# Optimization experiments

Hardware: AMD Instinct MI355X
Metric: run time of the kernel (lower is better)

## Reference

```python
import jax, jax.numpy as jnp
import numpy as np
import math

INPUT_FRAMES = 12
FUTURE_FRAMES = 26
T_STEPS = INPUT_FRAMES + FUTURE_FRAMES - 1  # 37
HD = 64   # hidden_dim
D = 16    # d_attn
CIN = 3   # input channels (time='stable')
COUT = 2  # output_dim
H, W = 24, 48


def conv2d(x, w, b, pad):
    # x: (N,C,H,W), w: (O,I,kh,kw)
    y = jax.lax.conv_general_dilated(x, w, (1, 1), [(pad, pad), (pad, pad)],
                                     dimension_numbers=('NCHW', 'OIHW', 'NCHW'))
    return y + b[None, :, None, None]


def spatial_attn(q, k, v):
    # q,k,v: (N,C,S); attention over spatial dim S
    scale = 1.0 / math.sqrt(q.shape[1])
    scores = jnp.einsum('ncs,nct->nst', q, k) * scale  # (N,S,S)
    a = jax.nn.softmax(scores, axis=-1)
    return jnp.einsum('nst,nct->ncs', a, v)


def setup_inputs() -> dict:
    key = jax.random.key(0)
    ks = jax.random.split(key, 8)
    s = 0.05
    inp = {
        'input_x': jax.random.normal(ks[0], (16, T_STEPS, H, W, CIN), dtype=jnp.float32),
        # ConvLSTM gate conv: in = CIN+HD, out = 4*HD, 3x3
        'conv_w': jax.random.normal(ks[1], (4 * HD, CIN + HD, 3, 3), dtype=jnp.float32) * s,
        'conv_b': jnp.zeros((4 * HD,), jnp.float32),
        # SA memory module
        'h_w': jax.random.normal(ks[2], (3 * D, HD, 1, 1), dtype=jnp.float32) * s,
        'h_b': jnp.zeros((3 * D,), jnp.float32),
        'm_w': jax.random.normal(ks[3], (2 * D, HD, 1, 1), dtype=jnp.float32) * s,
        'm_b': jnp.zeros((2 * D,), jnp.float32),
        'z_w': jax.random.normal(ks[4], (D, 2 * D, 1, 1), dtype=jnp.float32) * s,
        'z_b': jnp.zeros((D,), jnp.float32),
        'o_w': jax.random.normal(ks[5], (3 * HD, HD + D, 3, 3), dtype=jnp.float32) * s,
        'o_b': jnp.zeros((3 * HD,), jnp.float32),
        # final 1x1 projection to output_dim
        'out_w': jax.random.normal(ks[6], (COUT, HD, 1, 1), dtype=jnp.float32) * s,
        'out_b': jnp.zeros((COUT,), jnp.float32),
    }
    return inp


def reference(input_x, conv_w, conv_b, h_w, h_b, m_w, m_b, z_w, z_b, o_w, o_b, out_w, out_b):
    x = jnp.transpose(input_x, (0, 1, 4, 2, 3))  # (N,T,C,H,W)
    N = x.shape[0]
    S = H * W

    h0 = jnp.zeros((N, HD, H, W), x.dtype)
    carry0 = (h0, h0, h0, jnp.zeros((N, COUT, H, W), x.dtype))

    def step(carry, inp_t):
        h, c, m, prev_out = carry
        xt, t = inp_t  # xt: (N,CIN,H,W), t: scalar
        autoreg = jnp.concatenate([prev_out, xt[:, 2:]], axis=1)
        feed = jnp.where(t < INPUT_FRAMES, xt, autoreg)
        # ConvLSTM gates
        comb = conv2d(jnp.concatenate([feed, h], axis=1), conv_w, conv_b, 1)
        ci, cf, co, cg = jnp.split(comb, 4, axis=1)
        i = jax.nn.sigmoid(ci)
        f = jax.nn.sigmoid(cf)
        o = jax.nn.sigmoid(co)
        g = jnp.tanh(cg)
        c = f * c + i * g
        h = o * jnp.tanh(c)
        # self-attention memory
        hq, hk, hv = jnp.split(conv2d(h, h_w, h_b, 0), 3, axis=1)
        mk, mv = jnp.split(conv2d(m, m_w, m_b, 0), 2, axis=1)
        Zh = spatial_attn(hq.reshape(N, D, S), hk.reshape(N, D, S), hv.reshape(N, D, S))
        Zm = spatial_attn(hq.reshape(N, D, S), mk.reshape(N, D, S), mv.reshape(N, D, S))
        Z = conv2d(jnp.concatenate([Zh.reshape(N, D, H, W), Zm.reshape(N, D, H, W)], axis=1), z_w, z_b, 0)
        iog = conv2d(jnp.concatenate([Z, h], axis=1), o_w, o_b, 1)
        si, sg, so = jnp.split(iog, 3, axis=1)
        si = jax.nn.sigmoid(si)
        sg = jnp.tanh(sg)
        m = si * sg + (1.0 - si) * m
        h = jax.nn.sigmoid(so) * m
        out = conv2d(h, out_w, out_b, 0)
        return (h, c, m, out), out

    xs = (jnp.transpose(x, (1, 0, 2, 3, 4)), jnp.arange(T_STEPS))
    _, outs = jax.lax.scan(step, carry0, xs)
    outputs = jnp.transpose(outs, (1, 0, 2, 3, 4))  # (N,T,COUT,H,W)

    nino = outputs[:, -FUTURE_FRAMES:, 0, 10:13, 19:30].mean(axis=(2, 3))  # (N,26)
    nino_pred = (nino[:, :-2] + nino[:, 1:-1] + nino[:, 2:]) / 3.0          # (N,24)
    return outputs, nino_pred
```

## Files before the change

kernel.cpp:

```cpp
#include <hip/hip_runtime.h>
#include <math.h>

#define HD 64
#define DATT 16
#define NCIN 3
#define NCOUT 2
#define HH 24
#define WW 48
#define SS (HH*WW)
#define NB 16
#define TSTEPS 37
#define INPUT_FRAMES 12

#define PR 26
#define PC 52
#define PHW (PR*PC)

#define OFF_H     0
#define OFF_C     1384448
#define OFF_M     2564096
#define OFF_FEED  3743744
#define OFF_Z     3808640
#define ZERO_END  4154752
#define OFF_QKV   4154752
#define OFF_MKV   5039488
#define OFF_HB    5629312
#define OFF_IOG   8873344
#define OFF_BF2   12412288
#define OFF_BF    12596864

typedef __attribute__((ext_vector_type(8))) short short8;
typedef __attribute__((ext_vector_type(4))) float f32x4;

__device__ __forceinline__ float sigmoidf_(float x) {
    return 1.0f / (1.0f + __expf(-x));
}
__device__ __forceinline__ unsigned short f2bf(float f) {
    unsigned u = __float_as_uint(f);
    unsigned r = (u + 0x7fffu + ((u >> 16) & 1u)) >> 16;
    return (unsigned short)r;
}
__device__ __forceinline__ float bf2f(unsigned short b) {
    return __uint_as_float(((unsigned)b) << 16);
}
__device__ __forceinline__ unsigned packbf(float f) {
    unsigned short hi = f2bf(f);
    unsigned short lo = f2bf(f - bf2f(hi));
    return ((unsigned)lo << 16) | (unsigned)hi;
}
__device__ __forceinline__ float unpackbf(unsigned pk) {
    return __uint_as_float(pk << 16) + __uint_as_float(pk & 0xffff0000u);
}
__device__ __forceinline__ unsigned cvt_pk_bf16(float a, float b) {
    unsigned r;
    asm("v_cvt_pk_bf16_f32 %0, %1, %2" : "=v"(r) : "v"(a), "v"(b));
    return r;
}
__device__ __forceinline__ int permrow(int t) {
    int kb = t >> 5, tl = t & 31;
    int quad = tl >> 3, rr = tl & 7;
    return kb * 32 + ((rr >= 4) ? 16 : 0) + quad * 4 + (rr & 3);
}

#define MKFRAG(P0, P1, ah, al) do {                                  \
    ah.i[0] = (P0.y << 16) | (P0.x & 0xffff);                        \
    ah.i[1] = (P0.w << 16) | (P0.z & 0xffff);                        \
    ah.i[2] = (P1.y << 16) | (P1.x & 0xffff);                        \
    ah.i[3] = (P1.w << 16) | (P1.z & 0xffff);                        \
    al.i[0] = (P0.y & 0xffff0000) | ((unsigned)P0.x >> 16);          \
    al.i[1] = (P0.w & 0xffff0000) | ((unsigned)P0.z >> 16);          \
    al.i[2] = (P1.y & 0xffff0000) | ((unsigned)P1.x >> 16);          \
    al.i[3] = (P1.w & 0xffff0000) | ((unsigned)P1.z >> 16);          \
} while (0)

__global__ void k_zero(float* __restrict__ p, int n4) {
    int i = blockIdx.x * blockDim.x + threadIdx.x;
    if (i < n4) ((float4*)p)[i] = make_float4(0.f, 0.f, 0.f, 0.f);
}

__global__ void k_prep_bf2(const float* __restrict__ cw, unsigned short* __restrict__ bbuf) {
    int idx = blockIdx.x * 256 + threadIdx.x;
    if (idx >= 344064) return;
    int j    = idx & 7;
    int lane = (idx >> 3) & 63;
    int ki   = (idx >> 9) % 21;
    int nt   = (idx / 10752) % 16;
    int p    = idx / 172032;
    int k = ki * 32 + (lane >> 4) * 8 + j;
    int ncol = nt * 16 + (lane & 15);
    unsigned short v = 0;
    if (k < 648) {
        int c = k % 72, kt = k / 72;
        if (c < 67) {
            float w = cw[ncol * 603 + c * 9 + kt];
            unsigned short hi = f2bf(w);
            v = (p == 0) ? hi : f2bf(w - bf2f(hi));
        }
    }
    bbuf[idx] = v;
}

__global__ void k_prep_bf(const float* __restrict__ ow, unsigned short* __restrict__ bbuf) {
    int idx = blockIdx.x * 256 + threadIdx.x;
    if (idx >= 282624) return;
    int j    = idx & 7;
    int lane = (idx >> 3) & 63;
    int ki   = (idx >> 9) % 23;
    int nt   = (idx / 11776) % 12;
    int p    = idx / 141312;
    int k = ki * 32 + (lane >> 4) * 8 + j;
    int ncol = nt * 16 + (lane & 15);
    unsigned short v = 0;
    if (k < 720) {
        int c = k % 80, kt = k / 80;
        float w = ow[ncol * 720 + c * 9 + kt];
        unsigned short hi = f2bf(w);
        v = (p == 0) ? hi : f2bf(w - bf2f(hi));
    }
    bbuf[idx] = v;
}

__global__ void k_feed0(const float* __restrict__ x, unsigned* __restrict__ feed) {
    int i = blockIdx.x * blockDim.x + threadIdx.x;
    if (i >= NB * 3 * SS) return;
    int s = i % SS;
    int ch = (i / SS) % 3;
    int n = i / (3 * SS);
    int y = s / WW, xx = s % WW;
    float v = x[(((size_t)(n * TSTEPS + 0) * HH + y) * WW + xx) * NCIN + ch];
    feed[((size_t)(n * 3 + ch) * PR + (y + 1)) * PC + (xx + 1)] = packbf(v);
}

#define ASTR2 76
#define ZOFF2 (3*52*ASTR2)
__global__ __launch_bounds__(256) void k_conv_lstm_mfma(
    const unsigned* __restrict__ feed, const unsigned* __restrict__ hin,
    const unsigned short* __restrict__ bbuf, const float* __restrict__ cb,
    float* __restrict__ c, unsigned* __restrict__ hout)
{
    __shared__ __align__(16) int lds[3 * 52 * ASTR2 + 8];
    const int y0 = blockIdx.x;
    const int nb = blockIdx.y;
    const int n  = blockIdx.z;
    const int tid = threadIdx.x;

    const int ech = tid & 31;
    const int exg = tid >> 5;
    const int egch = nb * 32 + ech;
    const size_t ecbase = ((size_t)(n * HD + egch) * HH + y0) * WW + exg * 6;
    float cpre[6];
#pragma unroll
    for (int k = 0; k < 6; ++k) cpre[k] = c[ecbase + k];
    const float ebi = cb[egch], ebf = cb[64 + egch];
    const float ebo = cb[128 + egch], ebg = cb[192 + egch];

    const unsigned* fbase = feed + (size_t)n * 3 * PHW;
    const unsigned* hbase = hin + (size_t)n * HD * PHW;
    for (int e = tid; e < 2808; e += 256) {
        int grp = e / 156;
        int r2  = e - grp * 156;
        int pr = r2 / 52, pc = r2 - pr * 52;
        int cc0 = grp * 4;
        int vv[4];
#pragma unroll
        for (int j = 0; j < 4; ++j) {
            int cc = cc0 + j;
            int t = 0;
            if (cc < 3)        t = (int)fbase[(size_t)cc * PHW + (y0 + pr) * PC + pc];
            else if (cc < 67)  t = (int)hbase[(size_t)(cc - 3) * PHW + (y0 + pr) * PC + pc];
            vv[j] = t;
        }
        int4 v; v.x = vv[0]; v.y = vv[1]; v.z = vv[2]; v.w = vv[3];
        *(int4*)&lds[r2 * ASTR2 + cc0] = v;
    }
    if (tid < 8) lds[ZOFF2 + tid] = 0;
    __syncthreads();

    const int wv = tid >> 6;
    const int lane = tid & 63;
    const int mcol = lane & 15;
    const int quad = lane >> 4;

    f32x4 acc[2][3];
#pragma unroll
    for (int jg = 0; jg < 2; ++jg)
#pragma unroll
        for (int xt = 0; xt < 3; ++xt) acc[jg][xt] = (f32x4){0.f, 0.f, 0.f, 0.f};

    const unsigned short* b0 = bbuf + ((size_t)(wv * 4 + nb * 2 + 0) * 21) * 512 + lane * 8;
    const unsigned short* b1 = bbuf + ((size_t)(wv * 4 + nb * 2 + 1) * 21) * 512 + lane * 8;

    short8 cb0h = *(const short8*)(b0);
    short8 cb0l = *(const short8*)(b0 + 172032);
    short8 cb1h = *(const short8*)(b1);
    short8 cb1l = *(const short8*)(b1 + 172032);

    for (int ki = 0; ki < 21; ++ki) {
        int kn = (ki < 20) ? (ki + 1) * 512 : 20 * 512;
        short8 nb0h = *(const short8*)(b0 + kn);
        short8 nb0l = *(const short8*)(b0 + kn + 172032);
        short8 nb1h = *(const short8*)(b1 + kn);
        short8 nb1l = *(const short8*)(b1 + kn + 172032);

        int k0 = ki * 32 + quad * 8;
        int ab, step;
        if (k0 < 648) {
            int kt = k0 / 72;
            int c0 = k0 - kt * 72;
            int dy = kt / 3, dx = kt - dy * 3;
            ab = (dy * 52 + mcol + dx) * ASTR2 + c0;
            step = 16 * ASTR2;
        } else {
            ab = ZOFF2; step = 0;
        }
        int4 A0 = *(const int4*)&lds[ab],            A1 = *(const int4*)&lds[ab + 4];
        int4 B0 = *(const int4*)&lds[ab + step],     B1 = *(const int4*)&lds[ab + step + 4];
        int4 C0 = *(const int4*)&lds[ab + 2 * step], C1 = *(const int4*)&lds[ab + 2 * step + 4];

        union { int i[4]; short8 v; } ah, al;
        MKFRAG(A0, A1, ah, al);
        acc[0][0] = __builtin_amdgcn_mfma_f32_16x16x32_bf16(ah.v, cb0h, acc[0][0], 0, 0, 0);
        acc[0][0] = __builtin_amdgcn_mfma_f32_16x16x32_bf16(ah.v, cb0l, acc[0][0], 0, 0, 0);
        acc[0][0] = __builtin_amdgcn_mfma_f32_16x16x32_bf16(al.v, cb0h, acc[0][0], 0, 0, 0);
        acc[1][0] = __builtin_amdgcn_mfma_f32_16x16x32_bf16(ah.v, cb1h, acc[1][0], 0, 0, 0);
        acc[1][0] = __builtin_amdgcn_mfma_f32_16x16x32_bf16(ah.v, cb1l, acc[1][0], 0, 0, 0);
        acc[1][0] = __builtin_amdgcn_mfma_f32_16x16x32_bf16(al.v, cb1h, acc[1][0], 0, 0, 0);
        MKFRAG(B0, B1, ah, al);
        acc[0][1] = __builtin_amdgcn_mfma_f32_16x16x32_bf16(ah.v, cb0h, acc[0][1], 0, 0, 0);
        acc[0][1] = __builtin_amdgcn_mfma_f32_16x16x32_bf16(ah.v, cb0l, acc[0][1], 0, 0, 0);
        acc[0][1] = __builtin_amdgcn_mfma_f32_16x16x32_bf16(al.v, cb0h, acc[0][1], 0, 0, 0);
        acc[1][1] = __builtin_amdgcn_mfma_f32_16x16x32_bf16(ah.v, cb1h, acc[1][1], 0, 0, 0);
        acc[1][1] = __builtin_amdgcn_mfma_f32_16x16x32_bf16(ah.v, cb1l, acc[1][1], 0, 0, 0);
        acc[1][1] = __builtin_amdgcn_mfma_f32_16x16x32_bf16(al.v, cb1h, acc[1][1], 0, 0, 0);
        MKFRAG(C0, C1, ah, al);
        acc[0][2] = __builtin_amdgcn_mfma_f32_16x16x32_bf16(ah.v, cb0h, acc[0][2], 0, 0, 0);
        acc[0][2] = __builtin_amdgcn_mfma_f32_16x16x32_bf16(ah.v, cb0l, acc[0][2], 0, 0, 0);
        acc[0][2] = __builtin_amdgcn_mfma_f32_16x16x32_bf16(al.v, cb0h, acc[0][2], 0, 0, 0);
        acc[1][2] = __builtin_amdgcn_mfma_f32_16x16x32_bf16(ah.v, cb1h, acc[1][2], 0, 0, 0);
        acc[1][2] = __builtin_amdgcn_mfma_f32_16x16x32_bf16(ah.v, cb1l, acc[1][2], 0, 0, 0);
        acc[1][2] = __builtin_amdgcn_mfma_f32_16x16x32_bf16(al.v, cb1h, acc[1][2], 0, 0, 0);

        cb0h = nb0h; cb0l = nb0l; cb1h = nb1h; cb1l = nb1l;
    }

    __syncthreads();
    float* exch = (float*)lds;
#pragma unroll
    for (int jg = 0; jg < 2; ++jg)
#pragma unroll
        for (int xt = 0; xt < 3; ++xt)
#pragma unroll
            for (int r = 0; r < 4; ++r)
                exch[((wv * 2 + jg) * 3 + xt) * 272 + (quad * 4 + r) * 17 + mcol] = acc[jg][xt][r];
    __syncthreads();

    const int jg = ech >> 4, col = ech & 15;
    unsigned* hp = hout + ((size_t)(n * HD + egch) * PR + y0 + 1) * PC + 1;
#pragma unroll
    for (int k = 0; k < 6; ++k) {
        int x = exg * 6 + k;
        int xt = x >> 4, row = x & 15;
        float iv = sigmoidf_(exch[((0 * 2 + jg) * 3 + xt) * 272 + row * 17 + col] + ebi);
        float fv = sigmoidf_(exch[((1 * 2 + jg) * 3 + xt) * 272 + row * 17 + col] + ebf);
        float ov = sigmoidf_(exch[((2 * 2 + jg) * 3 + xt) * 272 + row * 17 + col] + ebo);
        float gv = tanhf    (exch[((3 * 2 + jg) * 3 + xt) * 272 + row * 17 + col] + ebg);
        float cn = fv * cpre[k] + iv * gv;
        float hn = ov * tanhf(cn);
        c[ecbase + k] = cn;
        hp[x] = packbf(hn);
    }
}

#define ASTR (84)
#define ZOFF (3*52*ASTR)
__global__ __launch_bounds__(192) void k_conv_sa(
    const unsigned* __restrict__ Zin, const unsigned* __restrict__ hin,
    const unsigned short* __restrict__ bbuf, const float* __restrict__ ob,
    float* __restrict__ m, unsigned* __restrict__ hout)
{
    __shared__ __align__(16) int lds[3 * 52 * ASTR + 8];
    const int y0 = blockIdx.x;
    const int cbk = blockIdx.y;
    const int n  = blockIdx.z;
    const int tid = threadIdx.x;

    const int ech = tid & 31;
    const int exg = tid >> 5;
    const int egch = cbk * 32 + ech;
    float* emrow = m + ((size_t)(n * HD + egch) * HH + y0) * WW;
    float mpre[8];
    {
        float4 a = *(const float4*)&emrow[exg * 8];
        float4 b = *(const float4*)&emrow[exg * 8 + 4];
        mpre[0] = a.x; mpre[1] = a.y; mpre[2] = a.z; mpre[3] = a.w;
        mpre[4] = b.x; mpre[5] = b.y; mpre[6] = b.z; mpre[7] = b.w;
    }
    const float ebsi = ob[egch], ebsg = ob[64 + egch], ebso = ob[128 + egch];

    const unsigned* zbase = Zin + (size_t)n * DATT * PHW;
    const unsigned* hbase = hin + (size_t)n * HD * PHW;
    for (int e = tid; e < 3120; e += 192) {
        int grp = e / 156;
        int r2  = e - grp * 156;
        int pr = r2 / 52, pc = r2 - pr * 52;
        int cc0 = grp * 4;
        int vv[4];
#pragma unroll
        for (int j = 0; j < 4; ++j) {
            int cc = cc0 + j;
            const unsigned* src = (cc < 16) ? (zbase + (size_t)cc * PHW)
                                            : (hbase + (size_t)(cc - 16) * PHW);
            vv[j] = (int)src[(y0 + pr) * PC + pc];
        }
        int4 v; v.x = vv[0]; v.y = vv[1]; v.z = vv[2]; v.w = vv[3];
        *(int4*)&lds[r2 * ASTR + cc0] = v;
    }
    if (tid < 8) lds[ZOFF + tid] = 0;
    __syncthreads();

    const int wv = tid >> 6;
    const int lane = tid & 63;
    const int mcol = lane & 15;
    const int quad = lane >> 4;

    f32x4 acc[2][3];
#pragma unroll
    for (int j = 0; j < 2; ++j)
#pragma unroll
        for (int xt = 0; xt < 3; ++xt) acc[j][xt] = (f32x4){0.f, 0.f, 0.f, 0.f};

    const unsigned short* b0 = bbuf + ((size_t)(wv * 4 + cbk * 2 + 0) * 23) * 512 + lane * 8;
    const unsigned short* b1 = bbuf + ((size_t)(wv * 4 + cbk * 2 + 1) * 23) * 512 + lane * 8;

    short8 cb0h = *(const short8*)(b0);
    short8 cb0l = *(const short8*)(b0 + 141312);
    short8 cb1h = *(const short8*)(b1);
    short8 cb1l = *(const short8*)(b1 + 141312);

    for (int ki = 0; ki < 23; ++ki) {
        int kn = (ki < 22) ? (ki + 1) * 512 : 22 * 512;
        short8 nb0h = *(const short8*)(b0 + kn);
        short8 nb0l = *(const short8*)(b0 + kn + 141312);
        short8 nb1h = *(const short8*)(b1 + kn);
        short8 nb1l = *(const short8*)(b1 + kn + 141312);

        int k0 = ki * 32 + quad * 8;
        int ab, step;
        if (k0 < 720) {
            int kt = k0 / 80;
            int c0 = k0 - kt * 80;
            int dy = kt / 3, dx = kt - dy * 3;
            ab = (dy * 52 + mcol + dx) * ASTR + c0;
            step = 16 * ASTR;
        } else {
            ab = ZOFF; step = 0;
        }
        int4 A0 = *(const int4*)&lds[ab],            A1 = *(const int4*)&lds[ab + 4];
        int4 B0 = *(const int4*)&lds[ab + step],     B1 = *(const int4*)&lds[ab + step + 4];
        int4 C0 = *(const int4*)&lds[ab + 2 * step], C1 = *(const int4*)&lds[ab + 2 * step + 4];

        union { int i[4]; short8 v; } ah, al;
        MKFRAG(A0, A1, ah, al);
        acc[0][0] = __builtin_amdgcn_mfma_f32_16x16x32_bf16(ah.v, cb0h, acc[0][0], 0, 0, 0);
        acc[0][0] = __builtin_amdgcn_mfma_f32_16x16x32_bf16(ah.v, cb0l, acc[0][0], 0, 0, 0);
        acc[0][0] = __builtin_amdgcn_mfma_f32_16x16x32_bf16(al.v, cb0h, acc[0][0], 0, 0, 0);
        acc[1][0] = __builtin_amdgcn_mfma_f32_16x16x32_bf16(ah.v, cb1h, acc[1][0], 0, 0, 0);
        acc[1][0] = __builtin_amdgcn_mfma_f32_16x16x32_bf16(ah.v, cb1l, acc[1][0], 0, 0, 0);
        acc[1][0] = __builtin_amdgcn_mfma_f32_16x16x32_bf16(al.v, cb1h, acc[1][0], 0, 0, 0);
        MKFRAG(B0, B1, ah, al);
        acc[0][1] = __builtin_amdgcn_mfma_f32_16x16x32_bf16(ah.v, cb0h, acc[0][1], 0, 0, 0);
        acc[0][1] = __builtin_amdgcn_mfma_f32_16x16x32_bf16(ah.v, cb0l, acc[0][1], 0, 0, 0);
        acc[0][1] = __builtin_amdgcn_mfma_f32_16x16x32_bf16(al.v, cb0h, acc[0][1], 0, 0, 0);
        acc[1][1] = __builtin_amdgcn_mfma_f32_16x16x32_bf16(ah.v, cb1h, acc[1][1], 0, 0, 0);
        acc[1][1] = __builtin_amdgcn_mfma_f32_16x16x32_bf16(ah.v, cb1l, acc[1][1], 0, 0, 0);
        acc[1][1] = __builtin_amdgcn_mfma_f32_16x16x32_bf16(al.v, cb1h, acc[1][1], 0, 0, 0);
        MKFRAG(C0, C1, ah, al);
        acc[0][2] = __builtin_amdgcn_mfma_f32_16x16x32_bf16(ah.v, cb0h, acc[0][2], 0, 0, 0);
        acc[0][2] = __builtin_amdgcn_mfma_f32_16x16x32_bf16(ah.v, cb0l, acc[0][2], 0, 0, 0);
        acc[0][2] = __builtin_amdgcn_mfma_f32_16x16x32_bf16(al.v, cb0h, acc[0][2], 0, 0, 0);
        acc[1][2] = __builtin_amdgcn_mfma_f32_16x16x32_bf16(ah.v, cb1h, acc[1][2], 0, 0, 0);
        acc[1][2] = __builtin_amdgcn_mfma_f32_16x16x32_bf16(ah.v, cb1l, acc[1][2], 0, 0, 0);
        acc[1][2] = __builtin_amdgcn_mfma_f32_16x16x32_bf16(al.v, cb1h, acc[1][2], 0, 0, 0);

        cb0h = nb0h; cb0l = nb0l; cb1h = nb1h; cb1l = nb1l;
    }

    __syncthreads();
    float* exch = (float*)lds;
#pragma unroll
    for (int j = 0; j < 2; ++j)
#pragma unroll
        for (int xt = 0; xt < 3; ++xt)
#pragma unroll
            for (int r = 0; r < 4; ++r)
                exch[((wv * 2 + j) * 3 + xt) * 272 + (quad * 4 + r) * 17 + mcol] = acc[j][xt][r];
    __syncthreads();

    const int jg = ech >> 4, col = ech & 15;
    unsigned* hp = hout + ((size_t)(n * HD + egch) * PR + y0 + 1) * PC + 1;
#pragma unroll
    for (int k = 0; k < 8; ++k) {
        int x = exg * 8 + k;
        int xt = x >> 4, row = x & 15;
        float si = sigmoidf_(exch[((0 * 2 + jg) * 3 + xt) * 272 + row * 17 + col] + ebsi);
        float sg = tanhf    (exch[((1 * 2 + jg) * 3 + xt) * 272 + row * 17 + col] + ebsg);
        float so =           exch[((2 * 2 + jg) * 3 + xt) * 272 + row * 17 + col] + ebso;
        float mn = si * sg + (1.f - si) * mpre[k];
        emrow[x] = mn;
        hp[x] = packbf(sigmoidf_(so) * mn);
    }
}

__global__ __launch_bounds__(256) void k_qkv(
    const unsigned* __restrict__ h, const float* __restrict__ m,
    const float* __restrict__ hw, const float* __restrict__ hb,
    const float* __restrict__ mw, const float* __restrict__ mb,
    unsigned short* __restrict__ pl) {
    __shared__ float lw[512];
    __shared__ float lb[8];
    const int g = blockIdx.y;
    const int tid = threadIdx.x;
    const float* wsrc = (g < 6) ? (hw + g * 512) : (mw + (g - 6) * 512);
    const float* bsrc = (g < 6) ? (hb + g * 8) : (mb + (g - 6) * 8);
    for (int i = tid; i < 512; i += 256) lw[i] = wsrc[i];
    if (tid < 8) lb[tid] = bsrc[tid];
    __syncthreads();

    int idx = blockIdx.x * 256 + tid;
    int s = idx % SS;
    int n = idx / SS;

    float reg[HD];
    if (g < 6) {
        int y = s / WW, x = s % WW;
        const unsigned* src = h + (size_t)n * HD * PHW + (y + 1) * PC + (x + 1);
#pragma unroll
        for (int ic = 0; ic < HD; ++ic) reg[ic] = unpackbf(src[ic * PHW]);
    } else {
        const float* src = m + (size_t)n * HD * SS + s;
#pragma unroll
        for (int ic = 0; ic < HD; ++ic) reg[ic] = src[ic * SS];
    }

    float out[8];
#pragma unroll
    for (int j = 0; j < 8; ++j) {
        const float* wr = &lw[j * HD];
        float a = lb[j];
#pragma unroll
        for (int ic = 0; ic < HD; ++ic) a += reg[ic] * wr[ic];
        out[j] = a;
    }

    unsigned short* bq  = pl;
    unsigned short* akh = pl + 294912;
    unsigned short* akm = pl + 589824;
    unsigned short* bvh = pl + 884736;
    unsigned short* bvm = pl + 1179648;
    const int c0 = (g & 1) * 8;

    if (g < 2) {
        unsigned w0 = (unsigned)f2bf(out[0]) | ((unsigned)f2bf(out[1]) << 16);
        unsigned w1 = (unsigned)f2bf(out[2]) | ((unsigned)f2bf(out[3]) << 16);
        unsigned w2 = (unsigned)f2bf(out[4]) | ((unsigned)f2bf(out[5]) << 16);
        unsigned w3 = (unsigned)f2bf(out[6]) | ((unsigned)f2bf(out[7]) << 16);
        *(uint4*)&bq[((size_t)n * SS + s) * 16 + c0] = make_uint4(w0, w1, w2, w3);
    } else if (g < 4 || (g >= 6 && g < 8)) {
        int row = permrow(s);
        unsigned short* base = (g < 4) ? akh : akm;
        unsigned w0 = (unsigned)f2bf(out[0]) | ((unsigned)f2bf(out[1]) << 16);
        unsigned w1 = (unsigned)f2bf(out[2]) | ((unsigned)f2bf(out[3]) << 16);
        unsigned w2 = (unsigned)f2bf(out[4]) | ((unsigned)f2bf(out[5]) << 16);
        unsigned w3 = (unsigned)f2bf(out[6]) | ((unsigned)f2bf(out[7]) << 16);
        *(uint4*)&base[((size_t)n * SS + row) * 16 + c0] = make_uint4(w0, w1, w2, w3);
    } else {
        unsigned short* base = (g < 6) ? bvh : bvm;
#pragma unroll
        for (int j = 0; j < 8; ++j)
            base[((size_t)n * 16 + c0 + j) * SS + s] = f2bf(out[j]);
    }
}

__global__ __launch_bounds__(256) void k_attn(
    const unsigned short* __restrict__ pl, const unsigned short* __restrict__ zbuf,
    const float* __restrict__ zw, const float* __restrict__ zb,
    unsigned* __restrict__ Z)
{
    __shared__ float ldsO[4][2][16][16];
    __shared__ float ldsF[2][16][16];
    __shared__ float ldsL[4][2][16];
    __shared__ float ldsLF[2][16];

    const int n   = blockIdx.x;
    const int qt  = blockIdx.y;
    const int tid = threadIdx.x;
    const int wv  = tid >> 6;
    const int lane = tid & 63;
    const int col  = lane & 15;
    const int quad = lane >> 4;
    const bool hi  = quad >= 2;

    const unsigned short* bq  = pl;
    const unsigned short* akh = pl + 294912;
    const unsigned short* akm = pl + 589824;
    const unsigned short* bvh = pl + 884736;
    const unsigned short* bvm = pl + 1179648;

    const size_t nb = (size_t)n * 18432;
    const int stepk = hi ? 0 : 512;
    const int subk  = hi ? 0 : 256;
    const unsigned short* qp  = hi ? zbuf : (bq  + nb + ((size_t)(qt * 16 + col)) * 16 + quad * 8);
    const unsigned short* khb = hi ? zbuf : (akh + nb + col * 16 + quad * 8);
    const unsigned short* kmb = hi ? zbuf : (akm + nb + col * 16 + quad * 8);
    const unsigned short* vhb = bvh + nb + (size_t)col * SS + quad * 8;
    const unsigned short* vmb = bvm + nb + (size_t)col * SS + quad * 8;

    short8 qf = *(const short8*)qp;

    f32x4 oh = (f32x4){0.f,0.f,0.f,0.f}, om = (f32x4){0.f,0.f,0.f,0.f};
    float lh = 0.f, lm = 0.f;
    const int kb0 = wv * 9, kb1 = kb0 + 9;
    for (int kb = kb0; kb < kb1; ++kb) {
        const unsigned short* kh0 = khb + (size_t)kb * stepk;
        const unsigned short* km0 = kmb + (size_t)kb * stepk;
        short8 khA = *(const short8*)kh0;
        short8 khB = *(const short8*)(kh0 + subk);
        short8 kmA = *(const short8*)km0;
        short8 kmB = *(const short8*)(km0 + subk);
        short8 vh  = *(const short8*)(vhb + (size_t)kb * 32);
        short8 vm  = *(const short8*)(vmb + (size_t)kb * 32);
        const f32x4 z4 = (f32x4){0.f,0.f,0.f,0.f};
        f32x4 sA = __builtin_amdgcn_mfma_f32_16x16x32_bf16(khA, qf, z4, 0, 0, 0);
        f32x4 sB = __builtin_amdgcn_mfma_f32_16x16x32_bf16(khB, qf, z4, 0, 0, 0);
        f32x4 tA = __builtin_amdgcn_mfma_f32_16x16x32_bf16(kmA, qf, z4, 0, 0, 0);
        f32x4 tB = __builtin_amdgcn_mfma_f32_16x16x32_bf16(kmB, qf, z4, 0, 0, 0);

        float pa0 = __expf(0.25f * sA[0]), pa1 = __expf(0.25f * sA[1]);
        float pa2 = __expf(0.25f * sA[2]), pa3 = __expf(0.25f * sA[3]);
        float pb0 = __expf(0.25f * sB[0]), pb1 = __expf(0.25f * sB[1]);
        float pb2 = __expf(0.25f * sB[2]), pb3 = __expf(0.25f * sB[3]);
        lh += (pa0 + pa1 + pa2 + pa3) + (pb0 + pb1 + pb2 + pb3);
        union { unsigned u[4]; short8 v; } ph;
        ph.u[0] = cvt_pk_bf16(pa0, pa1); ph.u[1] = cvt_pk_bf16(pa2, pa3);
        ph.u[2] = cvt_pk_bf16(pb0, pb1); ph.u[3] = cvt_pk_bf16(pb2, pb3);
        oh = __builtin_amdgcn_mfma_f32_16x16x32_bf16(ph.v, vh, oh, 0, 0, 0);

        float qa0 = __expf(0.25f * tA[0]), qa1 = __expf(0.25f * tA[1]);
        float qa2 = __expf(0.25f * tA[2]), qa3 = __expf(0.25f * tA[3]);
        float qb0 = __expf(0.25f * tB[0]), qb1 = __expf(0.25f * tB[1]);
        float qb2 = __expf(0.25f * tB[2]), qb3 = __expf(0.25f * tB[3]);
        lm += (qa0 + qa1 + qa2 + qa3) + (qb0 + qb1 + qb2 + qb3);
        union { unsigned u[4]; short8 v; } pm;
        pm.u[0] = cvt_pk_bf16(qa0, qa1); pm.u[1] = cvt_pk_bf16(qa2, qa3);
        pm.u[2] = cvt_pk_bf16(qb0, qb1); pm.u[3] = cvt_pk_bf16(qb2, qb3);
        om = __builtin_amdgcn_mfma_f32_16x16x32_bf16(pm.v, vm, om, 0, 0, 0);
    }

    lh += __shfl_xor(lh, 16); lh += __shfl_xor(lh, 32);
    lm += __shfl_xor(lm, 16); lm += __shfl_xor(lm, 32);

#pragma unroll
    for (int r = 0; r < 4; ++r) {
        ldsO[wv][0][quad * 4 + r][col] = oh[r];
        ldsO[wv][1][quad * 4 + r][col] = om[r];
    }
    if (lane < 16) { ldsL[wv][0][lane] = lh; ldsL[wv][1][lane] = lm; }
    __syncthreads();

    if (tid < 128) {
        int a_ = tid >> 6, rem = tid & 63, q_ = rem >> 2, j4 = (rem & 3) * 4;
        float4 s4 = make_float4(0.f, 0.f, 0.f, 0.f);
#pragma unroll
        for (int w = 0; w < 4; ++w) {
            float4 v = *(const float4*)&ldsO[w][a_][q_][j4];
            s4.x += v.x; s4.y += v.y; s4.z += v.z; s4.w += v.w;
        }
        *(float4*)&ldsF[a_][q_][j4] = s4;
    } else if (tid < 160) {
        int e = tid - 128, a_ = e >> 4, q_ = e & 15;
        ldsLF[a_][q_] = ldsL[0][a_][q_] + ldsL[1][a_][q_] +
                        ldsL[2][a_][q_] + ldsL[3][a_][q_];
    }
    __syncthreads();

    const int q  = tid & 15;
    const int zc = tid >> 4;
    float iLh = 1.f / ldsLF[0][q], iLm = 1.f / ldsLF[1][q];
    const float* zr = zw + zc * 32;
    float a = zb[zc];
#pragma unroll
    for (int j = 0; j < 16; ++j)
        a += zr[j] * (ldsF[0][q][j] * iLh) + zr[16 + j] * (ldsF[1][q][j] * iLm);
    int s = qt * 16 + q;
    int y = s / WW, x = s % WW;
    Z[((size_t)(n * DATT + zc) * PR + y + 1) * PC + x + 1] = packbf(a);
}

__global__ __launch_bounds__(256) void k_out_feed(
    const unsigned* __restrict__ h, const float* __restrict__ ow,
    const float* __restrict__ ob, const float* __restrict__ x,
    float* __restrict__ outbuf, unsigned* __restrict__ feed, int t) {
    const int tid = threadIdx.x;
    const int lane = tid & 63;
    const int wv = tid >> 6;
    const int part = lane >> 4;
    const int sl = lane & 15;
    int sidx = blockIdx.x * 64 + wv * 16 + sl;
    int s = sidx % SS;
    int n = sidx / SS;
    int y = s / WW, xx = s % WW;
    const unsigned* src = h + (size_t)n * HD * PHW + (y + 1) * PC + (xx + 1);
    float o0 = 0.f, o1 = 0.f;
#pragma unroll
    for (int i = 0; i < 16; ++i) {
        int ic = part * 16 + i;
        float r = unpackbf(src[ic * PHW]);
        o0 += r * ow[ic];
        o1 += r * ow[HD + ic];
    }
    o0 += __shfl_xor(o0, 16); o0 += __shfl_xor(o0, 32);
    o1 += __shfl_xor(o1, 16); o1 += __shfl_xor(o1, 32);

    if (part == 0) {
        o0 += ob[0]; o1 += ob[1];
        outbuf[(((size_t)n * TSTEPS + t) * NCOUT + 0) * SS + s] = o0;
        outbuf[(((size_t)n * TSTEPS + t) * NCOUT + 1) * SS + s] = o1;
        if (t + 1 < TSTEPS) {
            int t1 = t + 1;
            const float* xp = &x[(((size_t)(n * TSTEPS + t1) * HH + y) * WW + xx) * NCIN];
            float f0, f1, f2 = xp[2];
            if (t1 < INPUT_FRAMES) { f0 = xp[0]; f1 = xp[1]; }
            else { f0 = o0; f1 = o1; }
            size_t fb = ((size_t)(n * 3 + 0) * PR + y + 1) * PC + xx + 1;
            feed[fb] = packbf(f0);
            feed[fb + PHW] = packbf(f1);
            feed[fb + 2 * (size_t)PHW] = packbf(f2);
        }
    }
}

__global__ void k_nino(const float* __restrict__ outbuf, float* __restrict__ pred) {
    int tidx = threadIdx.x;
    if (tidx >= 16 * 24) return;
    int j = tidx % 24;
    int n = tidx / 24;
    float acc = 0.f;
    for (int f = j; f < j + 3; ++f) {
        int t = 11 + f;
        const float* p = &outbuf[(((size_t)n * TSTEPS + t) * NCOUT + 0) * SS];
        float sloc = 0.f;
        for (int y = 10; y <= 12; ++y)
            for (int x = 19; x <= 29; ++x)
                sloc += p[y * WW + x];
        acc += sloc * (1.f / 33.f);
    }
    pred[n * 24 + j] = acc * (1.f / 3.f);
}

extern "C" void kernel_launch(void* const* d_in, const int* in_sizes, int n_in,
                              void* d_out, int out_size, void* d_ws, size_t ws_size,
                              hipStream_t stream) {
    const float* x      = (const float*)d_in[0];
    const float* conv_w = (const float*)d_in[1];
    const float* conv_b = (const float*)d_in[2];
    const float* h_w    = (const float*)d_in[3];
    const float* h_b    = (const float*)d_in[4];
    const float* m_w    = (const float*)d_in[5];
    const float* m_b    = (const float*)d_in[6];
    const float* z_w    = (const float*)d_in[7];
    const float* z_b    = (const float*)d_in[8];
    const float* o_w    = (const float*)d_in[9];
    const float* o_b    = (const float*)d_in[10];
    const float* out_w  = (const float*)d_in[11];
    const float* out_b  = (const float*)d_in[12];

    float* ws   = (float*)d_ws;
    unsigned* hA    = (unsigned*)(ws + OFF_H);
    float* c    = ws + OFF_C;
    float* m    = ws + OFF_M;
    unsigned* feedp = (unsigned*)(ws + OFF_FEED);
    unsigned* Zp    = (unsigned*)(ws + OFF_Z);
    unsigned* hB    = (unsigned*)(ws + OFF_HB);
    unsigned short* bf2 = (unsigned short*)(ws + OFF_BF2);
    unsigned short* bf  = (unsigned short*)(ws + OFF_BF);
    unsigned short* planes = (unsigned short*)(ws + OFF_QKV);
    const unsigned short* zbuf = (const unsigned short*)(ws + OFF_MKV);
    float* outp = (float*)d_out;

    k_zero<<<4058, 256, 0, stream>>>(ws, 1038688);
    k_zero<<<1352, 256, 0, stream>>>(ws + OFF_HB, 346112);
    k_zero<<<1, 64, 0, stream>>>(ws + OFF_MKV, 16);
    k_prep_bf2<<<1344, 256, 0, stream>>>(conv_w, bf2);
    k_prep_bf<<<1104, 256, 0, stream>>>(o_w, bf);
    k_feed0<<<216, 256, 0, stream>>>(x, feedp);

    for (int t = 0; t < TSTEPS; ++t) {
        k_conv_lstm_mfma<<<dim3(24, 2, 16), 256, 0, stream>>>(feedp, hB, bf2, conv_b, c, hA);
        k_qkv<<<dim3(72, 10), 256, 0, stream>>>(hA, m, h_w, h_b, m_w, m_b, planes);
        k_attn<<<dim3(16, 72), 256, 0, stream>>>(planes, zbuf, z_w, z_b, Zp);
        k_conv_sa<<<dim3(24, 2, 16), 192, 0, stream>>>(Zp, hA, bf, o_b, m, hB);
        k_out_feed<<<288, 256, 0, stream>>>(hB, out_w, out_b, x, outp, feedp, t);
    }
    k_nino<<<1, 384, 0, stream>>>(outp, outp + (size_t)NB * TSTEPS * NCOUT * SS);
}
```

Measured before the change: 3.856 ms.

## Split K-loop of both conv MFMA kernels across two wave groups

Both implicit-GEMM conv kernels (ConvLSTM gate conv and SA output conv) now launch twice as many threads per block. Each pair of wave groups handles one half of the K reduction, and the partial sums are added during the LDS exchange before the gate nonlinearities. This targets latency and low occupancy in these kernels, which have only 768 blocks each, by raising waves per block. The cost is a larger LDS exchange buffer, extra adds and more register pressure under the new launch bounds.

```diff
diff --git a/kernel.cpp b/kernel.cpp
--- a/kernel.cpp
+++ b/kernel.cpp
@@ -133,12 +133,12 @@
 
 #define ASTR2 76
 #define ZOFF2 (3*52*ASTR2)
-__global__ __launch_bounds__(256) void k_conv_lstm_mfma(
+__global__ __launch_bounds__(512) void k_conv_lstm_mfma(
     const unsigned* __restrict__ feed, const unsigned* __restrict__ hin,
     const unsigned short* __restrict__ bbuf, const float* __restrict__ cb,
     float* __restrict__ c, unsigned* __restrict__ hout)
 {
-    __shared__ __align__(16) int lds[3 * 52 * ASTR2 + 8];
+    __shared__ __align__(16) int lds[13064];
     const int y0 = blockIdx.x;
     const int nb = blockIdx.y;
     const int n  = blockIdx.z;
@@ -147,16 +147,16 @@
     const int ech = tid & 31;
     const int exg = tid >> 5;
     const int egch = nb * 32 + ech;
-    const size_t ecbase = ((size_t)(n * HD + egch) * HH + y0) * WW + exg * 6;
-    float cpre[6];
-#pragma unroll
-    for (int k = 0; k < 6; ++k) cpre[k] = c[ecbase + k];
+    const size_t ecbase = ((size_t)(n * HD + egch) * HH + y0) * WW + exg * 3;
+    float cpre[3];
+#pragma unroll
+    for (int k = 0; k < 3; ++k) cpre[k] = c[ecbase + k];
     const float ebi = cb[egch], ebf = cb[64 + egch];
     const float ebo = cb[128 + egch], ebg = cb[192 + egch];
 
     const unsigned* fbase = feed + (size_t)n * 3 * PHW;
     const unsigned* hbase = hin + (size_t)n * HD * PHW;
-    for (int e = tid; e < 2808; e += 256) {
+    for (int e = tid; e < 2808; e += 512) {
         int grp = e / 156;
         int r2  = e - grp * 156;
         int pr = r2 / 52, pc = r2 - pr * 52;
@@ -177,6 +177,8 @@
     __syncthreads();
 
     const int wv = tid >> 6;
+    const int half = wv >> 2;
+    const int gate = wv & 3;
     const int lane = tid & 63;
     const int mcol = lane & 15;
     const int quad = lane >> 4;
@@ -187,16 +189,19 @@
 #pragma unroll
         for (int xt = 0; xt < 3; ++xt) acc[jg][xt] = (f32x4){0.f, 0.f, 0.f, 0.f};
 
-    const unsigned short* b0 = bbuf + ((size_t)(wv * 4 + nb * 2 + 0) * 21) * 512 + lane * 8;
-    const unsigned short* b1 = bbuf + ((size_t)(wv * 4 + nb * 2 + 1) * 21) * 512 + lane * 8;
-
-    short8 cb0h = *(const short8*)(b0);
-    short8 cb0l = *(const short8*)(b0 + 172032);
-    short8 cb1h = *(const short8*)(b1);
-    short8 cb1l = *(const short8*)(b1 + 172032);
-
-    for (int ki = 0; ki < 21; ++ki) {
-        int kn = (ki < 20) ? (ki + 1) * 512 : 20 * 512;
+    const unsigned short* b0 = bbuf + ((size_t)(gate * 4 + nb * 2 + 0) * 21) * 512 + lane * 8;
+    const unsigned short* b1 = bbuf + ((size_t)(gate * 4 + nb * 2 + 1) * 21) * 512 + lane * 8;
+
+    const int ki0 = half ? 11 : 0;
+    const int ki1 = half ? 21 : 11;
+
+    short8 cb0h = *(const short8*)(b0 + ki0 * 512);
+    short8 cb0l = *(const short8*)(b0 + ki0 * 512 + 172032);
+    short8 cb1h = *(const short8*)(b1 + ki0 * 512);
+    short8 cb1l = *(const short8*)(b1 + ki0 * 512 + 172032);
+
+    for (int ki = ki0; ki < ki1; ++ki) {
+        int kn = (ki + 1 < ki1) ? (ki + 1) * 512 : ki * 512;
         short8 nb0h = *(const short8*)(b0 + kn);
         short8 nb0l = *(const short8*)(b0 + kn + 172032);
         short8 nb1h = *(const short8*)(b1 + kn);
@@ -251,29 +256,32 @@
         for (int xt = 0; xt < 3; ++xt)
 #pragma unroll
             for (int r = 0; r < 4; ++r)
-                exch[((wv * 2 + jg) * 3 + xt) * 272 + (quad * 4 + r) * 17 + mcol] = acc[jg][xt][r];
+                exch[(((half * 4 + gate) * 2 + jg) * 3 + xt) * 272 + (quad * 4 + r) * 17 + mcol]
+                    = acc[jg][xt][r];
     __syncthreads();
 
     const int jg = ech >> 4, col = ech & 15;
     unsigned* hp = hout + ((size_t)(n * HD + egch) * PR + y0 + 1) * PC + 1;
-#pragma unroll
-    for (int k = 0; k < 6; ++k) {
-        int x = exg * 6 + k;
+#define EXL(hf, g) exch[((((hf) * 4 + (g)) * 2 + jg) * 3 + xt) * 272 + row * 17 + col]
+#pragma unroll
+    for (int k = 0; k < 3; ++k) {
+        int x = exg * 3 + k;
         int xt = x >> 4, row = x & 15;
-        float iv = sigmoidf_(exch[((0 * 2 + jg) * 3 + xt) * 272 + row * 17 + col] + ebi);
-        float fv = sigmoidf_(exch[((1 * 2 + jg) * 3 + xt) * 272 + row * 17 + col] + ebf);
-        float ov = sigmoidf_(exch[((2 * 2 + jg) * 3 + xt) * 272 + row * 17 + col] + ebo);
-        float gv = tanhf    (exch[((3 * 2 + jg) * 3 + xt) * 272 + row * 17 + col] + ebg);
+        float iv = sigmoidf_(EXL(0, 0) + EXL(1, 0) + ebi);
+        float fv = sigmoidf_(EXL(0, 1) + EXL(1, 1) + ebf);
+        float ov = sigmoidf_(EXL(0, 2) + EXL(1, 2) + ebo);
+        float gv = tanhf    (EXL(0, 3) + EXL(1, 3) + ebg);
         float cn = fv * cpre[k] + iv * gv;
         float hn = ov * tanhf(cn);
         c[ecbase + k] = cn;
         hp[x] = packbf(hn);
     }
+#undef EXL
 }
 
 #define ASTR (84)
 #define ZOFF (3*52*ASTR)
-__global__ __launch_bounds__(192) void k_conv_sa(
+__global__ __launch_bounds__(384) void k_conv_sa(
     const unsigned* __restrict__ Zin, const unsigned* __restrict__ hin,
     const unsigned short* __restrict__ bbuf, const float* __restrict__ ob,
     float* __restrict__ m, unsigned* __restrict__ hout)
@@ -288,18 +296,16 @@
     const int exg = tid >> 5;
     const int egch = cbk * 32 + ech;
     float* emrow = m + ((size_t)(n * HD + egch) * HH + y0) * WW;
-    float mpre[8];
+    float mpre[4];
     {
-        float4 a = *(const float4*)&emrow[exg * 8];
-        float4 b = *(const float4*)&emrow[exg * 8 + 4];
+        float4 a = *(const float4*)&emrow[exg * 4];
         mpre[0] = a.x; mpre[1] = a.y; mpre[2] = a.z; mpre[3] = a.w;
-        mpre[4] = b.x; mpre[5] = b.y; mpre[6] = b.z; mpre[7] = b.w;
     }
     const float ebsi = ob[egch], ebsg = ob[64 + egch], ebso = ob[128 + egch];
 
     const unsigned* zbase = Zin + (size_t)n * DATT * PHW;
     const unsigned* hbase = hin + (size_t)n * HD * PHW;
-    for (int e = tid; e < 3120; e += 192) {
+    for (int e = tid; e < 3120; e += 384) {
         int grp = e / 156;
         int r2  = e - grp * 156;
         int pr = r2 / 52, pc = r2 - pr * 52;
@@ -319,6 +325,8 @@
     __syncthreads();
 
     const int wv = tid >> 6;
+    const int half = (wv >= 3) ? 1 : 0;
+    const int gate = wv - half * 3;
     const int lane = tid & 63;
     const int mcol = lane & 15;
     const int quad = lane >> 4;
@@ -329,16 +337,19 @@
 #pragma unroll
         for (int xt = 0; xt < 3; ++xt) acc[j][xt] = (f32x4){0.f, 0.f, 0.f, 0.f};
 
-    const unsigned short* b0 = bbuf + ((size_t)(wv * 4 + cbk * 2 + 0) * 23) * 512 + lane * 8;
-    const unsigned short* b1 = bbuf + ((size_t)(wv * 4 + cbk * 2 + 1) * 23) * 512 + lane * 8;
-
-    short8 cb0h = *(const short8*)(b0);
-    short8 cb0l = *(const short8*)(b0 + 141312);
-    short8 cb1h = *(const short8*)(b1);
-    short8 cb1l = *(const short8*)(b1 + 141312);
-
-    for (int ki = 0; ki < 23; ++ki) {
-        int kn = (ki < 22) ? (ki + 1) * 512 : 22 * 512;
+    const unsigned short* b0 = bbuf + ((size_t)(gate * 4 + cbk * 2 + 0) * 23) * 512 + lane * 8;
+    const unsigned short* b1 = bbuf + ((size_t)(gate * 4 + cbk * 2 + 1) * 23) * 512 + lane * 8;
+
+    const int ki0 = half ? 12 : 0;
+    const int ki1 = half ? 23 : 12;
+
+    short8 cb0h = *(const short8*)(b0 + ki0 * 512);
+    short8 cb0l = *(const short8*)(b0 + ki0 * 512 + 141312);
+    short8 cb1h = *(const short8*)(b1 + ki0 * 512);
+    short8 cb1l = *(const short8*)(b1 + ki0 * 512 + 141312);
+
+    for (int ki = ki0; ki < ki1; ++ki) {
+        int kn = (ki + 1 < ki1) ? (ki + 1) * 512 : ki * 512;
         short8 nb0h = *(const short8*)(b0 + kn);
         short8 nb0l = *(const short8*)(b0 + kn + 141312);
         short8 nb1h = *(const short8*)(b1 + kn);
@@ -393,22 +404,25 @@
         for (int xt = 0; xt < 3; ++xt)
 #pragma unroll
             for (int r = 0; r < 4; ++r)
-                exch[((wv * 2 + j) * 3 + xt) * 272 + (quad * 4 + r) * 17 + mcol] = acc[j][xt][r];
+                exch[(((half * 3 + gate) * 2 + j) * 3 + xt) * 272 + (quad * 4 + r) * 17 + mcol]
+                    = acc[j][xt][r];
     __syncthreads();
 
     const int jg = ech >> 4, col = ech & 15;
     unsigned* hp = hout + ((size_t)(n * HD + egch) * PR + y0 + 1) * PC + 1;
-#pragma unroll
-    for (int k = 0; k < 8; ++k) {
-        int x = exg * 8 + k;
+#define EXS(hf, g) exch[((((hf) * 3 + (g)) * 2 + jg) * 3 + xt) * 272 + row * 17 + col]
+#pragma unroll
+    for (int k = 0; k < 4; ++k) {
+        int x = exg * 4 + k;
         int xt = x >> 4, row = x & 15;
-        float si = sigmoidf_(exch[((0 * 2 + jg) * 3 + xt) * 272 + row * 17 + col] + ebsi);
-        float sg = tanhf    (exch[((1 * 2 + jg) * 3 + xt) * 272 + row * 17 + col] + ebsg);
-        float so =           exch[((2 * 2 + jg) * 3 + xt) * 272 + row * 17 + col] + ebso;
+        float si = sigmoidf_(EXS(0, 0) + EXS(1, 0) + ebsi);
+        float sg = tanhf    (EXS(0, 1) + EXS(1, 1) + ebsg);
+        float so =           EXS(0, 2) + EXS(1, 2) + ebso;
         float mn = si * sg + (1.f - si) * mpre[k];
         emrow[x] = mn;
         hp[x] = packbf(sigmoidf_(so) * mn);
     }
+#undef EXS
 }
 
 __global__ __launch_bounds__(256) void k_qkv(
@@ -695,10 +709,10 @@
     k_feed0<<<216, 256, 0, stream>>>(x, feedp);
 
     for (int t = 0; t < TSTEPS; ++t) {
-        k_conv_lstm_mfma<<<dim3(24, 2, 16), 256, 0, stream>>>(feedp, hB, bf2, conv_b, c, hA);
+        k_conv_lstm_mfma<<<dim3(24, 2, 16), 512, 0, stream>>>(feedp, hB, bf2, conv_b, c, hA);
         k_qkv<<<dim3(72, 10), 256, 0, stream>>>(hA, m, h_w, h_b, m_w, m_b, planes);
         k_attn<<<dim3(16, 72), 256, 0, stream>>>(planes, zbuf, z_w, z_b, Zp);
-        k_conv_sa<<<dim3(24, 2, 16), 192, 0, stream>>>(Zp, hA, bf, o_b, m, hB);
+        k_conv_sa<<<dim3(24, 2, 16), 384, 0, stream>>>(Zp, hA, bf, o_b, m, hB);
         k_out_feed<<<288, 256, 0, stream>>>(hB, out_w, out_b, x, outp, feedp, t);
     }
     k_nino<<<1, 384, 0, stream>>>(outp, outp + (size_t)NB * TSTEPS * NCOUT * SS);
```

After: 3.985 ms. 1.03x slower.
